# Performance work log

Measured on AMD Instinct MI355X. Metric: run time of the kernel, lower is better.

## Reference

```python
import jax, jax.numpy as jnp
import numpy as np

N_QUBITS = 8
N_QLAYERS = 2
D_MODEL = 8
NUM_HEADS = 2
DEPTH = D_MODEL // NUM_HEADS


def _apply_1q(state, U, wire):
    # state: (T, 2, 2, ..., 2); U: (2, 2) complex
    state = jnp.moveaxis(state, 1 + wire, -1)
    state = jnp.einsum('...b,ab->...a', state, U)
    return jnp.moveaxis(state, -1, 1 + wire)


def _apply_cnot(state, ctrl, tgt):
    s = jnp.moveaxis(state, (1 + ctrl, 1 + tgt), (-2, -1))
    s = jnp.concatenate([s[..., :1, :], s[..., 1:, ::-1]], axis=-2)
    return jnp.moveaxis(s, (-2, -1), (1 + ctrl, 1 + tgt))


def _z_signs(n):
    idx = jnp.arange(2 ** n)
    bits = (idx[:, None] >> jnp.arange(n - 1, -1, -1)[None, :]) & 1  # col i = qubit i
    return (1.0 - 2.0 * bits).astype(jnp.float32)  # (2^n, n)


def quantum_circuit(x, w):
    """AngleEmbedding(RX) + BasicEntanglerLayers(RX + CNOT ring) + PauliZ expvals.
    x: (T, n) float angles; w: (L, n) float weights -> (T, n) float expvals."""
    T, n = x.shape
    L = w.shape[0]
    # AngleEmbedding: RX(x_i)|0> = cos(x_i/2)|0> - i sin(x_i/2)|1>; product state
    h = 0.5 * x
    amps = jnp.stack([jnp.cos(h).astype(jnp.complex64),
                      (-1j) * jnp.sin(h).astype(jnp.complex64)], axis=-1)  # (T, n, 2)
    state = amps[:, 0, :]
    for i in range(1, n):
        state = (state[:, :, None] * amps[:, i, None, :]).reshape(T, -1)
    state = state.reshape((T,) + (2,) * n)
    for l in range(L):
        for i in range(n):
            th = 0.5 * w[l, i]
            cc = jnp.cos(th).astype(jnp.complex64)
            ss = (-1j) * jnp.sin(th).astype(jnp.complex64)
            U = jnp.stack([jnp.stack([cc, ss]), jnp.stack([ss, cc])])  # RX(w)
            state = _apply_1q(state, U, i)
        pairs = [(i, (i + 1) % n) for i in range(n)] if n > 2 else [(0, 1)]
        for c, t in pairs:
            state = _apply_cnot(state, c, t)
    probs = jnp.abs(state.reshape(T, -1)) ** 2  # (T, 2^n)
    return probs @ _z_signs(n)  # (T, n)


def setup_inputs() -> dict:
    key = jax.random.key(0)
    ks = jax.random.split(key, 8)
    B, S, d = 32, 1024, D_MODEL
    q = jax.random.normal(ks[0], (B, S, d), dtype=jnp.float32)
    k = jax.random.normal(ks[1], (B, S, d), dtype=jnp.float32)
    v = jax.random.normal(ks[2], (B, S, d), dtype=jnp.float32)
    mask = jnp.triu(jnp.ones((S, S), dtype=jnp.float32), k=1)[None, None]  # causal
    weights_q = jax.random.uniform(ks[3], (N_QLAYERS, N_QUBITS), dtype=jnp.float32, maxval=2 * np.pi)
    weights_k = jax.random.uniform(ks[4], (N_QLAYERS, N_QUBITS), dtype=jnp.float32, maxval=2 * np.pi)
    weights_v = jax.random.uniform(ks[5], (N_QLAYERS, N_QUBITS), dtype=jnp.float32, maxval=2 * np.pi)
    weights_dense = jax.random.uniform(ks[6], (N_QLAYERS, N_QUBITS), dtype=jnp.float32, maxval=2 * np.pi)
    return {"q": q, "k": k, "v": v, "mask": mask,
            "weights_q": weights_q, "weights_k": weights_k,
            "weights_v": weights_v, "weights_dense": weights_dense}


def reference(q, k, v, mask, weights_q, weights_k, weights_v, weights_dense):
    B, S, d = q.shape
    T = B * S
    # per-token quantum Q/K/V embeddings (batched over all B*S tokens)
    qe = quantum_circuit(q.reshape(T, d), weights_q).reshape(B, S, d)
    ke = quantum_circuit(k.reshape(T, d), weights_k).reshape(B, S, d)
    ve = quantum_circuit(v.reshape(T, d), weights_v).reshape(B, S, d)
    # split heads: (B, H, S, depth)
    def split(x):
        return x.reshape(B, S, NUM_HEADS, DEPTH).transpose(0, 2, 1, 3)
    qh, kh, vh = split(qe), split(ke), split(ve)
    scores = jnp.einsum('bhqd,bhkd->bhqk', qh, kh) / jnp.sqrt(jnp.float32(DEPTH))
    scores = scores + mask * (-1e9)
    attn = jax.nn.softmax(scores, axis=-1)
    ctx = jnp.einsum('bhqk,bhkd->bhqd', attn, vh)
    ctx = ctx.transpose(0, 2, 1, 3).reshape(B, S, d)
    out = quantum_circuit(ctx.reshape(T, d), weights_dense).reshape(B, S, d)
    return out, attn
```

## Files before the change

kernel.cpp:

```cpp
#include <hip/hip_runtime.h>

#define S_LEN 1024
#define BATCH 32
#define NHEAD 2
#define HDIM  4


#define TBL_STRIDE 256

__global__ __launch_bounds__(256)
void pauli_setup(const float* __restrict__ wq, const float* __restrict__ wk,
                 const float* __restrict__ wv, const float* __restrict__ wd,
                 float4* __restrict__ tables, int* __restrict__ counts)
{
    int blk = blockIdx.x;
    int set = blk >> 3, w = blk & 7;
    const float* wt = (set == 0) ? wq : (set == 1) ? wk : (set == 2) ? wv : wd;

    float c2[8], s2[8];
#pragma unroll
    for (int j = 0; j < 8; ++j) {
        float th = wt[8 + j];
        s2[j] = __sinf(th);
        c2[j] = __cosf(th);
    }

    unsigned X = 0u, Z = 1u << w;
    int sg0 = 0;
#pragma unroll
    for (int g = 7; g >= 0; --g) {
        int c = g, t = (g + 1) & 7;
        unsigned xc = (X >> c) & 1u, zt = (Z >> t) & 1u;
        unsigned xt = (X >> t) & 1u, zc = (Z >> c) & 1u;
        sg0 ^= (int)(xc & zt & (xt ^ zc ^ 1u));
        X ^= xc << t;
        Z ^= zt << c;
    }

    int tid = threadIdx.x;
    float coef = sg0 ? -1.0f : 1.0f;
    unsigned Xb = X;
    int k = 0;
#pragma unroll
    for (int j = 0; j < 8; ++j) {
        if ((Z >> j) & 1u) {
            int bit = (tid >> k) & 1;
            ++k;
            if (!((X >> j) & 1u)) {
                if (bit) { Xb |= 1u << j; coef *= s2[j]; }
                else     { coef *= c2[j]; }
            } else {
                if (bit) { Xb &= ~(1u << j); coef *= -s2[j]; }
                else     { coef *= c2[j]; }
            }
        }
    }
    bool valid = (tid < (1 << k));

    unsigned Xf = Xb, Zf = Z;
    int sg = 0;
#pragma unroll
    for (int g = 7; g >= 0; --g) {
        int c = g, t = (g + 1) & 7;
        unsigned xc = (Xf >> c) & 1u, zt = (Zf >> t) & 1u;
        unsigned xt = (Xf >> t) & 1u, zc = (Zf >> c) & 1u;
        sg ^= (int)(xc & zt & (xt ^ zc ^ 1u));
        Xf ^= xc << t;
        Zf ^= zt << c;
    }

    bool keep = valid && ((Xf & ~Zf) == 0u);
    if (sg ^ (__popc(Xf) & 1)) coef = -coef;
    unsigned zonly = Zf & ~Xf;
    unsigned ymask = Xf;

    __shared__ int wsum[4];
    int lane = tid & 63, wvx = tid >> 6;
    unsigned long long mb = __ballot((int)keep);
    if (lane == 0) wsum[wvx] = __popcll(mb);
    __syncthreads();
    int prefix = 0;
#pragma unroll
    for (int i = 0; i < 4; ++i)
        if (i < wvx) prefix += wsum[i];
    int pos = prefix + __popcll(mb & ((1ull << lane) - 1ull));
    if (keep) {
        float4 t4;
        t4.x = __int_as_float((int)zonly);
        t4.y = __int_as_float((int)ymask);
        t4.z = coef;
        t4.w = 0.0f;
        tables[blk * TBL_STRIDE + pos] = t4;
    }
    __syncthreads();
    if (tid == 0) counts[blk] = wsum[0] + wsum[1] + wsum[2] + wsum[3];
}

__global__ __launch_bounds__(256)
void qc_eval(const float* __restrict__ x0, const float* __restrict__ w0a,
             const float* __restrict__ x1, const float* __restrict__ w0b,
             const float* __restrict__ x2, const float* __restrict__ w0c,
             const float4* __restrict__ tables, const int* __restrict__ counts,
             float* __restrict__ o0, float* __restrict__ o1, float* __restrict__ o2,
             int rows_per_seg, int set_base)
{
    int gtid = blockIdx.x * 256 + threadIdx.x;
    int rowg = gtid >> 2;
    int op   = gtid & 3;
    int seg  = rowg / rows_per_seg;
    int row  = rowg - seg * rows_per_seg;
    const float* x  = (seg == 0) ? x0 : (seg == 1) ? x1 : x2;
    const float* w0 = (seg == 0) ? w0a : (seg == 1) ? w0b : w0c;
    float*       o  = (seg == 0) ? o0 : (seg == 1) ? o1 : o2;
    int set = set_base + seg;

    const float4* xp = reinterpret_cast<const float4*>(x + (size_t)row * 8);
    float4 xa = xp[0], xb = xp[1];
    float cc[8], ss[8];
    {
        float a;
        a = xa.x + w0[0]; __sincosf(a, &ss[0], &cc[0]);
        a = xa.y + w0[1]; __sincosf(a, &ss[1], &cc[1]);
        a = xa.z + w0[2]; __sincosf(a, &ss[2], &cc[2]);
        a = xa.w + w0[3]; __sincosf(a, &ss[3], &cc[3]);
        a = xb.x + w0[4]; __sincosf(a, &ss[4], &cc[4]);
        a = xb.y + w0[5]; __sincosf(a, &ss[5], &cc[5]);
        a = xb.z + w0[6]; __sincosf(a, &ss[6], &cc[6]);
        a = xb.w + w0[7]; __sincosf(a, &ss[7], &cc[7]);
    }

    const int wA4[4] = {0, 2, 3, 4};
    const int wB4[4] = {1, 7, 6, 5};
    int wA = wA4[op], wB = wB4[op];

#pragma unroll
    for (int half = 0; half < 2; ++half) {
        int w = half ? wB : wA;
        int blk = set * 8 + w;
        int cnt = counts[blk];
        const float4* base = tables + blk * TBL_STRIDE;
        float acc = 0.0f;
        for (int t = 0; t < cnt; ++t) {
            float4 T = base[t];
            unsigned zm = (unsigned)__float_as_int(T.x);
            unsigned ym = (unsigned)__float_as_int(T.y);
            float v = T.z;
#pragma unroll
            for (int m = 0; m < 8; ++m) {
                float f = ((ym >> m) & 1u) ? ss[m]
                        : (((zm >> m) & 1u) ? cc[m] : 1.0f);
                v *= f;
            }
            acc += v;
        }
        o[(size_t)row * 8 + w] = acc;
    }
}

template <int CTRL>
__device__ __forceinline__ float dpp_acc(float x)
{
    int y = __builtin_amdgcn_update_dpp(0, __float_as_int(x), CTRL, 0xf, 0xf, false);
    return x + __int_as_float(y);
}

__device__ __forceinline__ float wave_reduce63(float x)
{
    x = dpp_acc<0x111>(x);
    x = dpp_acc<0x112>(x);
    x = dpp_acc<0x114>(x);
    x = dpp_acc<0x118>(x);
    x = dpp_acc<0x142>(x);
    x = dpp_acc<0x143>(x);
    return x;
}

__device__ __forceinline__ float bcast63(float x)
{
    return __int_as_float(__builtin_amdgcn_readlane(__float_as_int(x), 63));
}

__global__ __launch_bounds__(256)
void attn_kernel(const float* qe, const float* __restrict__ ke,
                 const float* __restrict__ ve, float* __restrict__ attn,
                 float* ctx)
{
    __shared__ float4 kc[4][S_LEN / 4];
    __shared__ float4 vc[4][S_LEN / 4];

    int tid = threadIdx.x;
    int bid = blockIdx.x;
    int it  = bid & 15;
    int h   = (bid >> 4) & 1;
    int b   = bid >> 5;
    int lane = tid & 63;
    int wave = tid >> 6;

    const float4* ke4 = reinterpret_cast<const float4*>(ke) + h;
    const float4* ve4 = reinterpret_cast<const float4*>(ve) + h;
    size_t rowbase = (size_t)b * S_LEN;

    for (int j = tid; j < S_LEN; j += 256) {
        kc[j & 3][j >> 2] = ke4[(rowbase + j) * 2];
        vc[j & 3][j >> 2] = ve4[(rowbase + j) * 2];
    }
    __syncthreads();

    int i0 = it * 64 + wave * 16;
    const float* qp = qe + (rowbase + i0) * 8 + h * HDIM;
    float4* attn4 = reinterpret_cast<float4*>(attn);
    size_t head4 = ((size_t)(b * NHEAD + h)) * S_LEN * (S_LEN / 4);

    for (int pr = 0; pr < 8; ++pr) {
        int i = i0 + pr * 2;

        float4 qa = *reinterpret_cast<const float4*>(qp + pr * 16);
        float4 qb = *reinterpret_cast<const float4*>(qp + pr * 16 + 8);
        qa.x *= 0.5f; qa.y *= 0.5f; qa.z *= 0.5f; qa.w *= 0.5f;
        qb.x *= 0.5f; qb.y *= 0.5f; qb.z *= 0.5f; qb.w *= 0.5f;

        float pea[16], peb[16];
        float suma = 0.0f, sumb = 0.0f;
        float4 pva = {0, 0, 0, 0}, pvb = {0, 0, 0, 0};

#pragma unroll
        for (int t = 0; t < 4; ++t) {
            int m = t * 64 + lane;
            int jb = m << 2;
#pragma unroll
            for (int c = 0; c < 4; ++c) {
                float4 kk = kc[c][m];
                float4 vv = vc[c][m];
                float sa = qa.x * kk.x + qa.y * kk.y + qa.z * kk.z + qa.w * kk.w;
                float sb = qb.x * kk.x + qb.y * kk.y + qb.z * kk.z + qb.w * kk.w;
                int j = jb + c;
                float pa = (j <= i)     ? __expf(sa) : 0.0f;
                float pb = (j <= i + 1) ? __expf(sb) : 0.0f;
                pea[t * 4 + c] = pa;
                peb[t * 4 + c] = pb;
                suma += pa; sumb += pb;
                pva.x += pa * vv.x; pva.y += pa * vv.y;
                pva.z += pa * vv.z; pva.w += pa * vv.w;
                pvb.x += pb * vv.x; pvb.y += pb * vv.y;
                pvb.z += pb * vv.z; pvb.w += pb * vv.w;
            }
        }

        float inva = 1.0f / bcast63(wave_reduce63(suma));
        float invb = 1.0f / bcast63(wave_reduce63(sumb));

        size_t base4 = head4 + (size_t)i * (S_LEN / 4) + lane;
#pragma unroll
        for (int t = 0; t < 4; ++t) {
            float4 oa, ob;
            oa.x = pea[t * 4 + 0] * inva; oa.y = pea[t * 4 + 1] * inva;
            oa.z = pea[t * 4 + 2] * inva; oa.w = pea[t * 4 + 3] * inva;
            ob.x = peb[t * 4 + 0] * invb; ob.y = peb[t * 4 + 1] * invb;
            ob.z = peb[t * 4 + 2] * invb; ob.w = peb[t * 4 + 3] * invb;
            attn4[base4 + t * 64] = oa;
            attn4[base4 + (S_LEN / 4) + t * 64] = ob;
        }

        pva.x = wave_reduce63(pva.x); pva.y = wave_reduce63(pva.y);
        pva.z = wave_reduce63(pva.z); pva.w = wave_reduce63(pva.w);
        pvb.x = wave_reduce63(pvb.x); pvb.y = wave_reduce63(pvb.y);
        pvb.z = wave_reduce63(pvb.z); pvb.w = wave_reduce63(pvb.w);

        if (lane == 63) {
            float* cp = ctx + (rowbase + i) * 8 + h * HDIM;
            cp[0]  = pva.x * inva; cp[1]  = pva.y * inva;
            cp[2]  = pva.z * inva; cp[3]  = pva.w * inva;
            cp[8]  = pvb.x * invb; cp[9]  = pvb.y * invb;
            cp[10] = pvb.z * invb; cp[11] = pvb.w * invb;
        }
    }
}

extern "C" void kernel_launch(void* const* d_in, const int* in_sizes, int n_in,
                              void* d_out, int out_size, void* d_ws, size_t ws_size,
                              hipStream_t stream)
{
    const float* q  = (const float*)d_in[0];
    const float* k  = (const float*)d_in[1];
    const float* v  = (const float*)d_in[2];
    const float* wq = (const float*)d_in[4];
    const float* wk = (const float*)d_in[5];
    const float* wv = (const float*)d_in[6];
    const float* wd = (const float*)d_in[7];

    float* out  = (float*)d_out;
    float* attn = out + (size_t)BATCH * S_LEN * 8;

    float*  ws     = (float*)d_ws;
    float*  qe     = ws;
    float*  ke     = ws + 262144;
    float*  ve     = ws + 524288;
    float4* tables = (float4*)(ws + 786432);
    int*    counts = (int*)(ws + 786432 + 32768);

    const int rows = BATCH * S_LEN;

    pauli_setup<<<dim3(32), 256, 0, stream>>>(wq, wk, wv, wd, tables, counts);

    qc_eval<<<dim3(rows * 3 * 4 / 256), 256, 0, stream>>>(
        q, wq, k, wk, v, wv, tables, counts, qe, ke, ve, rows, 0);

    attn_kernel<<<dim3(BATCH * NHEAD * 16), 256, 0, stream>>>(qe, ke, ve, attn, qe);

    qc_eval<<<dim3(rows * 4 / 256), 256, 0, stream>>>(
        qe, wd, qe, wd, qe, wd, tables, counts, out, out, out, rows, 3);
}
```

Before: 89.51 us.

## Fuse attention and dense quantum circuit into one kernel over both heads

Attention now runs with 512-thread blocks that handle both heads of a batch/query tile. The per-row context is staged in shared memory, and the final dense-layer Pauli-table circuit evaluation runs in the same kernel. This drops one kernel launch and the global round trip of the context buffer. In exchange, shared memory per block doubles and only half as many blocks are launched, which may reduce occupancy and parallelism.

```diff
diff --git a/kernel.cpp b/kernel.cpp
--- a/kernel.cpp
+++ b/kernel.cpp
@@ -180,36 +180,42 @@
     return __int_as_float(__builtin_amdgcn_readlane(__float_as_int(x), 63));
 }
 
-__global__ __launch_bounds__(256)
-void attn_kernel(const float* qe, const float* __restrict__ ke,
-                 const float* __restrict__ ve, float* __restrict__ attn,
-                 float* ctx)
-{
-    __shared__ float4 kc[4][S_LEN / 4];
-    __shared__ float4 vc[4][S_LEN / 4];
+__global__ __launch_bounds__(512)
+void attn_fused(const float* __restrict__ qe, const float* __restrict__ ke,
+                const float* __restrict__ ve, const float* __restrict__ wd,
+                const float4* __restrict__ tables, const int* __restrict__ counts,
+                float* __restrict__ attn, float* __restrict__ out)
+{
+    __shared__ float4 kc[2][4][S_LEN / 4];
+    __shared__ float4 vc[2][4][S_LEN / 4];
+    __shared__ float  ctxL[64][9];
 
     int tid = threadIdx.x;
     int bid = blockIdx.x;
     int it  = bid & 15;
-    int h   = (bid >> 4) & 1;
-    int b   = bid >> 5;
+    int b   = bid >> 4;
     int lane = tid & 63;
     int wave = tid >> 6;
-
-    const float4* ke4 = reinterpret_cast<const float4*>(ke) + h;
-    const float4* ve4 = reinterpret_cast<const float4*>(ve) + h;
+    int hw   = wave >> 2;
+    int wg   = wave & 3;
+
+    const float4* ke4 = reinterpret_cast<const float4*>(ke);
+    const float4* ve4 = reinterpret_cast<const float4*>(ve);
     size_t rowbase = (size_t)b * S_LEN;
 
-    for (int j = tid; j < S_LEN; j += 256) {
-        kc[j & 3][j >> 2] = ke4[(rowbase + j) * 2];
-        vc[j & 3][j >> 2] = ve4[(rowbase + j) * 2];
+    for (int j = tid; j < S_LEN; j += 512) {
+        size_t idx = (rowbase + j) * 2;
+        kc[0][j & 3][j >> 2] = ke4[idx];
+        kc[1][j & 3][j >> 2] = ke4[idx + 1];
+        vc[0][j & 3][j >> 2] = ve4[idx];
+        vc[1][j & 3][j >> 2] = ve4[idx + 1];
     }
     __syncthreads();
 
-    int i0 = it * 64 + wave * 16;
-    const float* qp = qe + (rowbase + i0) * 8 + h * HDIM;
+    int i0 = it * 64 + wg * 16;
+    const float* qp = qe + (rowbase + i0) * 8 + hw * HDIM;
     float4* attn4 = reinterpret_cast<float4*>(attn);
-    size_t head4 = ((size_t)(b * NHEAD + h)) * S_LEN * (S_LEN / 4);
+    size_t head4 = ((size_t)(b * NHEAD + hw)) * S_LEN * (S_LEN / 4);
 
     for (int pr = 0; pr < 8; ++pr) {
         int i = i0 + pr * 2;
@@ -229,8 +235,8 @@
             int jb = m << 2;
 #pragma unroll
             for (int c = 0; c < 4; ++c) {
-                float4 kk = kc[c][m];
-                float4 vv = vc[c][m];
+                float4 kk = kc[hw][c][m];
+                float4 vv = vc[hw][c][m];
                 float sa = qa.x * kk.x + qa.y * kk.y + qa.z * kk.z + qa.w * kk.w;
                 float sb = qb.x * kk.x + qb.y * kk.y + qb.z * kk.z + qb.w * kk.w;
                 int j = jb + c;
@@ -267,12 +273,46 @@
         pvb.z = wave_reduce63(pvb.z); pvb.w = wave_reduce63(pvb.w);
 
         if (lane == 63) {
-            float* cp = ctx + (rowbase + i) * 8 + h * HDIM;
-            cp[0]  = pva.x * inva; cp[1]  = pva.y * inva;
-            cp[2]  = pva.z * inva; cp[3]  = pva.w * inva;
-            cp[8]  = pvb.x * invb; cp[9]  = pvb.y * invb;
-            cp[10] = pvb.z * invb; cp[11] = pvb.w * invb;
-        }
+            int r0 = wg * 16 + pr * 2;
+            ctxL[r0][hw * 4 + 0]     = pva.x * inva;
+            ctxL[r0][hw * 4 + 1]     = pva.y * inva;
+            ctxL[r0][hw * 4 + 2]     = pva.z * inva;
+            ctxL[r0][hw * 4 + 3]     = pva.w * inva;
+            ctxL[r0 + 1][hw * 4 + 0] = pvb.x * invb;
+            ctxL[r0 + 1][hw * 4 + 1] = pvb.y * invb;
+            ctxL[r0 + 1][hw * 4 + 2] = pvb.z * invb;
+            ctxL[r0 + 1][hw * 4 + 3] = pvb.w * invb;
+        }
+    }
+    __syncthreads();
+
+    {
+        int r = tid >> 3;
+        int w = tid & 7;
+        float cc[8], ss[8];
+#pragma unroll
+        for (int m = 0; m < 8; ++m) {
+            float a = ctxL[r][m] + wd[m];
+            __sincosf(a, &ss[m], &cc[m]);
+        }
+        int blk = 24 + w;
+        int cnt = counts[blk];
+        const float4* base = tables + blk * TBL_STRIDE;
+        float acc = 0.0f;
+        for (int t = 0; t < cnt; ++t) {
+            float4 T = base[t];
+            unsigned zm = (unsigned)__float_as_int(T.x);
+            unsigned ym = (unsigned)__float_as_int(T.y);
+            float v = T.z;
+#pragma unroll
+            for (int m = 0; m < 8; ++m) {
+                float f = ((ym >> m) & 1u) ? ss[m]
+                        : (((zm >> m) & 1u) ? cc[m] : 1.0f);
+                v *= f;
+            }
+            acc += v;
+        }
+        out[(rowbase + it * 64 + r) * 8 + w] = acc;
     }
 }
 
@@ -305,8 +345,6 @@
     qc_eval<<<dim3(rows * 3 * 4 / 256), 256, 0, stream>>>(
         q, wq, k, wk, v, wv, tables, counts, qe, ke, ve, rows, 0);
 
-    attn_kernel<<<dim3(BATCH * NHEAD * 16), 256, 0, stream>>>(qe, ke, ve, attn, qe);
-
-    qc_eval<<<dim3(rows * 4 / 256), 256, 0, stream>>>(
-        qe, wd, qe, wd, qe, wd, tables, counts, out, out, out, rows, 3);
-}
+    attn_fused<<<dim3(BATCH * 16), 512, 0, stream>>>(
+        qe, ke, ve, wd, tables, counts, attn, out);
+}
```

New measurement: 89.81 us. About the same (+0.3%).

## Skip masked causal tiles in attention and split zero-fill into dedicated blocks

Applied to the files above, without the earlier changes.

Attention blocks now only load K/V and compute exp/softmax up to the causal limit of their 64-row tile, skipping fully masked 256-column chunks. Separate blocks, interleaved 4 compute to 3 zero-fill in a grid of 1792, write zeros into the masked upper-triangle region of the attention output. Each wave now processes one query row at a time instead of two. This removes wasted exp and arithmetic on masked entries and balances the zero-store traffic across extra blocks. The cost is more blocks, some index division, and less per-row instruction-level parallelism.

```diff
diff --git a/kernel.cpp b/kernel.cpp
--- a/kernel.cpp
+++ b/kernel.cpp
@@ -190,17 +190,46 @@
 
     int tid = threadIdx.x;
     int bid = blockIdx.x;
-    int it  = bid & 15;
-    int h   = (bid >> 4) & 1;
-    int b   = bid >> 5;
+    int g   = bid / 7;
+    int r   = bid - g * 7;
+    float4* attn4 = reinterpret_cast<float4*>(attn);
+    const float4 zero4 = make_float4(0.0f, 0.0f, 0.0f, 0.0f);
+
+    if (r >= 4) {
+        int zidx = g * 3 + (r - 4);
+        int it   = zidx % 12;
+        int rest = zidx / 12;
+        int h    = rest & 1;
+        int b    = rest >> 1;
+        int tmax = (it >> 2) + 1;
+        int c04  = tmax * 64;
+        int nc4  = 256 - c04;
+        size_t head4 = ((size_t)(b * NHEAD + h)) * S_LEN * (S_LEN / 4)
+                     + (size_t)(it * 64) * (S_LEN / 4);
+        int total = 64 * nc4;
+        for (int idx = tid; idx < total; idx += 256) {
+            int row = idx / nc4;
+            int col = idx - row * nc4;
+            attn4[head4 + (size_t)row * (S_LEN / 4) + c04 + col] = zero4;
+        }
+        return;
+    }
+
+    int cidx = g * 4 + r;
+    int it  = cidx & 15;
+    int h   = (cidx >> 4) & 1;
+    int b   = cidx >> 5;
     int lane = tid & 63;
     int wave = tid >> 6;
+
+    int tmax = (it >> 2) + 1;
+    int jmax = tmax << 8;
 
     const float4* ke4 = reinterpret_cast<const float4*>(ke) + h;
     const float4* ve4 = reinterpret_cast<const float4*>(ve) + h;
     size_t rowbase = (size_t)b * S_LEN;
 
-    for (int j = tid; j < S_LEN; j += 256) {
+    for (int j = tid; j < jmax; j += 256) {
         kc[j & 3][j >> 2] = ke4[(rowbase + j) * 2];
         vc[j & 3][j >> 2] = ve4[(rowbase + j) * 2];
     }
@@ -208,70 +237,56 @@
 
     int i0 = it * 64 + wave * 16;
     const float* qp = qe + (rowbase + i0) * 8 + h * HDIM;
-    float4* attn4 = reinterpret_cast<float4*>(attn);
     size_t head4 = ((size_t)(b * NHEAD + h)) * S_LEN * (S_LEN / 4);
 
-    for (int pr = 0; pr < 8; ++pr) {
-        int i = i0 + pr * 2;
-
-        float4 qa = *reinterpret_cast<const float4*>(qp + pr * 16);
-        float4 qb = *reinterpret_cast<const float4*>(qp + pr * 16 + 8);
-        qa.x *= 0.5f; qa.y *= 0.5f; qa.z *= 0.5f; qa.w *= 0.5f;
-        qb.x *= 0.5f; qb.y *= 0.5f; qb.z *= 0.5f; qb.w *= 0.5f;
-
-        float pea[16], peb[16];
-        float suma = 0.0f, sumb = 0.0f;
-        float4 pva = {0, 0, 0, 0}, pvb = {0, 0, 0, 0};
+    for (int rr = 0; rr < 16; ++rr) {
+        int i = i0 + rr;
+
+        float4 qv = *reinterpret_cast<const float4*>(qp + rr * 8);
+        qv.x *= 0.5f; qv.y *= 0.5f; qv.z *= 0.5f; qv.w *= 0.5f;
+
+        float pe[16];
+        float sum = 0.0f;
+        float4 pv = {0, 0, 0, 0};
 
 #pragma unroll
         for (int t = 0; t < 4; ++t) {
+            if (t >= tmax) continue;
             int m = t * 64 + lane;
             int jb = m << 2;
 #pragma unroll
             for (int c = 0; c < 4; ++c) {
                 float4 kk = kc[c][m];
                 float4 vv = vc[c][m];
-                float sa = qa.x * kk.x + qa.y * kk.y + qa.z * kk.z + qa.w * kk.w;
-                float sb = qb.x * kk.x + qb.y * kk.y + qb.z * kk.z + qb.w * kk.w;
+                float s = qv.x * kk.x + qv.y * kk.y + qv.z * kk.z + qv.w * kk.w;
                 int j = jb + c;
-                float pa = (j <= i)     ? __expf(sa) : 0.0f;
-                float pb = (j <= i + 1) ? __expf(sb) : 0.0f;
-                pea[t * 4 + c] = pa;
-                peb[t * 4 + c] = pb;
-                suma += pa; sumb += pb;
-                pva.x += pa * vv.x; pva.y += pa * vv.y;
-                pva.z += pa * vv.z; pva.w += pa * vv.w;
-                pvb.x += pb * vv.x; pvb.y += pb * vv.y;
-                pvb.z += pb * vv.z; pvb.w += pb * vv.w;
+                float p = (j <= i) ? __expf(s) : 0.0f;
+                pe[t * 4 + c] = p;
+                sum += p;
+                pv.x += p * vv.x; pv.y += p * vv.y;
+                pv.z += p * vv.z; pv.w += p * vv.w;
             }
         }
 
-        float inva = 1.0f / bcast63(wave_reduce63(suma));
-        float invb = 1.0f / bcast63(wave_reduce63(sumb));
+        float inv = 1.0f / bcast63(wave_reduce63(sum));
 
         size_t base4 = head4 + (size_t)i * (S_LEN / 4) + lane;
 #pragma unroll
         for (int t = 0; t < 4; ++t) {
-            float4 oa, ob;
-            oa.x = pea[t * 4 + 0] * inva; oa.y = pea[t * 4 + 1] * inva;
-            oa.z = pea[t * 4 + 2] * inva; oa.w = pea[t * 4 + 3] * inva;
-            ob.x = peb[t * 4 + 0] * invb; ob.y = peb[t * 4 + 1] * invb;
-            ob.z = peb[t * 4 + 2] * invb; ob.w = peb[t * 4 + 3] * invb;
-            attn4[base4 + t * 64] = oa;
-            attn4[base4 + (S_LEN / 4) + t * 64] = ob;
-        }
-
-        pva.x = wave_reduce63(pva.x); pva.y = wave_reduce63(pva.y);
-        pva.z = wave_reduce63(pva.z); pva.w = wave_reduce63(pva.w);
-        pvb.x = wave_reduce63(pvb.x); pvb.y = wave_reduce63(pvb.y);
-        pvb.z = wave_reduce63(pvb.z); pvb.w = wave_reduce63(pvb.w);
+            if (t >= tmax) continue;
+            float4 o;
+            o.x = pe[t * 4 + 0] * inv; o.y = pe[t * 4 + 1] * inv;
+            o.z = pe[t * 4 + 2] * inv; o.w = pe[t * 4 + 3] * inv;
+            attn4[base4 + t * 64] = o;
+        }
+
+        pv.x = wave_reduce63(pv.x); pv.y = wave_reduce63(pv.y);
+        pv.z = wave_reduce63(pv.z); pv.w = wave_reduce63(pv.w);
 
         if (lane == 63) {
             float* cp = ctx + (rowbase + i) * 8 + h * HDIM;
-            cp[0]  = pva.x * inva; cp[1]  = pva.y * inva;
-            cp[2]  = pva.z * inva; cp[3]  = pva.w * inva;
-            cp[8]  = pvb.x * invb; cp[9]  = pvb.y * invb;
-            cp[10] = pvb.z * invb; cp[11] = pvb.w * invb;
+            cp[0] = pv.x * inv; cp[1] = pv.y * inv;
+            cp[2] = pv.z * inv; cp[3] = pv.w * inv;
         }
     }
 }
@@ -305,7 +320,7 @@
     qc_eval<<<dim3(rows * 3 * 4 / 256), 256, 0, stream>>>(
         q, wq, k, wk, v, wv, tables, counts, qe, ke, ve, rows, 0);
 
-    attn_kernel<<<dim3(BATCH * NHEAD * 16), 256, 0, stream>>>(qe, ke, ve, attn, qe);
+    attn_kernel<<<dim3(1792), 256, 0, stream>>>(qe, ke, ve, attn, qe);
 
     qc_eval<<<dim3(rows * 4 / 256), 256, 0, stream>>>(
         qe, wd, qe, wd, qe, wd, tables, counts, out, out, out, rows, 3);
```

New measurement: 98.55 us. +10.1%, slower.
